# Optimization experiments

Measured on AMD Instinct MI355X. Metric: run time of the kernel, lower is better.

Reference implementation:

```python
import jax, jax.numpy as jnp
import numpy as np

STAGE = 100  # number of weight bins


def _bin_reconstruct(w, affine):
    # Faithful vectorization of the 100-iter binning loop: element in bin i
    # (half-open interval) gets scaled by affine[i]; the max element falls
    # outside every bin (w < wmin + stage*range/stage fails) and is zeroed.
    flat = w.reshape(-1)
    wmin, wmax = flat.min(), flat.max()
    idx = jnp.floor((flat - wmin) / (wmax - wmin) * STAGE).astype(jnp.int32)
    mask = (idx < STAGE).astype(flat.dtype)  # mask is detached in torch (non-diff anyway)
    scale = affine[jnp.clip(idx, 0, STAGE - 1)]
    return flat * scale * mask


def _kl_vs_laplace(new_flat, lap):
    # F.kl_div(log_softmax(w), softmax(lap), reduction='none').mean()
    logq = jax.nn.log_softmax(new_flat)
    p = jax.nn.softmax(lap)
    return (p * (jnp.log(p) - logq)).mean()


def _adder2d(x, w, stride, padding, groups=1):
    # AdderNet conv: out = -sum_k |patch_k - w_k| (no bias)
    O, Cg, kh, kw = w.shape
    patches = jax.lax.conv_general_dilated_patches(
        x, (kh, kw), (stride, stride), [(padding, padding), (padding, padding)])
    B, _, Hp, Wp = patches.shape  # channel dim ordered (C, kh, kw), C-major
    if groups == 1:
        p = patches.reshape(B, 1, Cg * kh * kw, Hp, Wp)
        wf = w.reshape(1, O, Cg * kh * kw, 1, 1)
    else:  # depthwise: groups == C_in, Cg == 1, O == C_in
        p = patches.reshape(B, O, kh * kw, Hp, Wp)
        wf = w.reshape(1, O, kh * kw, 1, 1)
    return -jnp.abs(p - wf).sum(axis=2)  # [B, O, Hp, Wp]


def _bn_train(x, g, b, eps=1e-5):
    # BatchNorm2d in training mode (batch statistics, biased variance)
    m = x.mean(axis=(0, 2, 3), keepdims=True)
    v = ((x - m) ** 2).mean(axis=(0, 2, 3), keepdims=True)
    return (x - m) * jax.lax.rsqrt(v + eps) * g.reshape(1, -1, 1, 1) + b.reshape(1, -1, 1, 1)


def _forward(x, sw_ds, sw_c1, sw_c2, sw_c3, a_ds, a_c1, a_c2, a_c3, peg_w,
             g1, b1, g2, b2, g3, b3, gds, bds, lap_ds, lap_c1, lap_c2, lap_c3):
    kl = jnp.float32(0.0)
    f_ds = _bin_reconstruct(sw_ds, a_ds)
    kl = kl + _kl_vs_laplace(f_ds, lap_ds)
    f_c1 = _bin_reconstruct(sw_c1, a_c1)
    kl = kl + _kl_vs_laplace(f_c1, lap_c1)
    residual = jax.nn.relu(_bn_train(_adder2d(x, f_ds.reshape(sw_ds.shape), 1, 0), gds, bds))
    h = _adder2d(x, f_c1.reshape(sw_c1.shape), 1, 0)
    h = _adder2d(h, peg_w, 1, 1, groups=peg_w.shape[0])  # PEG depthwise 3x3
    h = jax.nn.relu(_bn_train(h, g1, b1))
    f_c2 = _bin_reconstruct(sw_c2, a_c2)
    kl = kl + _kl_vs_laplace(f_c2, lap_c2)
    h = _adder2d(h, f_c2.reshape(sw_c2.shape), 1, 1)
    h = jax.nn.relu(_bn_train(h, g2, b2))
    f_c3 = _bin_reconstruct(sw_c3, a_c3)
    kl = kl + _kl_vs_laplace(f_c3, lap_c3)
    h = _adder2d(h, f_c3.reshape(sw_c3.shape), 1, 0)
    h = _bn_train(h, g3, b3)  # bn3 gamma zero-initialized
    return jax.nn.relu(h + residual), kl


def setup_inputs() -> dict:
    key = jax.random.key(0)
    ks = jax.random.split(key, 16)
    inp = {
        'x': jax.random.normal(ks[0], (4, 128, 28, 28), jnp.float32),
        'sw_downsample': jax.random.normal(ks[1], (256, 128, 1, 1), jnp.float32) * 0.05,
        'sw_conv1': jax.random.normal(ks[2], (64, 128, 1, 1), jnp.float32) * 0.05,
        'sw_conv2': jax.random.normal(ks[3], (64, 64, 3, 3), jnp.float32) * 0.05,
        'sw_conv3': jax.random.normal(ks[4], (256, 64, 1, 1), jnp.float32) * 0.05,
        'downsample_affine': jax.random.normal(ks[5], (100,), jnp.float32),
        'conv1_affine': jax.random.normal(ks[6], (100,), jnp.float32),
        'conv2_affine': jax.random.normal(ks[7], (100,), jnp.float32),
        'conv3_affine': jax.random.normal(ks[8], (100,), jnp.float32),
        'peg_w': jax.random.normal(ks[9], (64, 1, 3, 3), jnp.float32) * 0.05,
        'bn1_g': jnp.ones((64,), jnp.float32), 'bn1_b': jnp.zeros((64,), jnp.float32),
        'bn2_g': jnp.ones((64,), jnp.float32), 'bn2_b': jnp.zeros((64,), jnp.float32),
        'bn3_g': jnp.zeros((256,), jnp.float32), 'bn3_b': jnp.zeros((256,), jnp.float32),
        'bnds_g': jnp.ones((256,), jnp.float32), 'bnds_b': jnp.zeros((256,), jnp.float32),
        # Laplace(0, 2) samples, drawn once in setup so the reference is deterministic
        'lap_ds': jax.random.laplace(ks[10], (32768,), jnp.float32) * 2.0,
        'lap_c1': jax.random.laplace(ks[11], (8192,), jnp.float32) * 2.0,
        'lap_c2': jax.random.laplace(ks[12], (36864,), jnp.float32) * 2.0,
        'lap_c3': jax.random.laplace(ks[13], (16384,), jnp.float32) * 2.0,
    }
    return inp


def reference(x, sw_downsample, sw_conv1, sw_conv2, sw_conv3,
              downsample_affine, conv1_affine, conv2_affine, conv3_affine, peg_w,
              bn1_g, bn1_b, bn2_g, bn2_b, bn3_g, bn3_b, bnds_g, bnds_b,
              lap_ds, lap_c1, lap_c2, lap_c3):
    return _forward(x, sw_downsample, sw_conv1, sw_conv2, sw_conv3,
                    downsample_affine, conv1_affine, conv2_affine, conv3_affine, peg_w,
                    bn1_g, bn1_b, bn2_g, bn2_b, bn3_g, bn3_b, bnds_g, bnds_b,
                    lap_ds, lap_c1, lap_c2, lap_c3)
```

## Files before the change

kernel.cpp:

```cpp
#include <hip/hip_runtime.h>
#include <math.h>


#define HW 784
#define NB 4
#define STAGE 100

__device__ __forceinline__ float wredSum(float v){
  for (int o = 32; o > 0; o >>= 1) v += __shfl_down(v, o, 64);
  return v;
}
__device__ __forceinline__ float wredMax(float v){
  for (int o = 32; o > 0; o >>= 1) v = fmaxf(v, __shfl_down(v, o, 64));
  return v;
}
__device__ __forceinline__ float wredMin(float v){
  for (int o = 32; o > 0; o >>= 1) v = fminf(v, __shfl_down(v, o, 64));
  return v;
}
__device__ __forceinline__ double wredSumD(double v){
  for (int o = 32; o > 0; o >>= 1) v += __shfl_down(v, o, 64);
  return v;
}

__device__ float blockMin4(float v){
  __shared__ float shn[4];
  __syncthreads();
  v = wredMin(v);
  if ((threadIdx.x & 63) == 0) shn[threadIdx.x >> 6] = v;
  __syncthreads();
  return fminf(fminf(shn[0], shn[1]), fminf(shn[2], shn[3]));
}
__device__ float blockMax4(float v){
  __shared__ float shx[4];
  __syncthreads();
  v = wredMax(v);
  if ((threadIdx.x & 63) == 0) shx[threadIdx.x >> 6] = v;
  __syncthreads();
  return fmaxf(fmaxf(shx[0], shx[1]), fmaxf(shx[2], shx[3]));
}

__device__ void stats4(float v0, float v1, float v2, float v3,
                       double* sumP, double* sqP, int oc0){
  __shared__ double sred[4][8];
  __syncthreads();
  const int w = threadIdx.x >> 6;
  float vv[4] = {v0, v1, v2, v3};
  #pragma unroll
  for (int i = 0; i < 4; i++){
    double d = (double)vv[i];
    double s = wredSumD(d);
    double q = wredSumD(d * d);
    if ((threadIdx.x & 63) == 0){ sred[w][i] = s; sred[w][4 + i] = q; }
  }
  __syncthreads();
  if (threadIdx.x < 8){
    double tot = sred[0][threadIdx.x] + sred[1][threadIdx.x]
               + sred[2][threadIdx.x] + sred[3][threadIdx.x];
    int i = threadIdx.x & 3;
    if (threadIdx.x < 4) atomicAdd(&sumP[oc0 + i], tot);
    else                 atomicAdd(&sqP[oc0 + i],  tot);
  }
}
__device__ void stats2(float v0, float v1, double* sumP, double* sqP, int oc0){
  __shared__ double sred2[4][4];
  __syncthreads();
  const int w = threadIdx.x >> 6;
  float vv[2] = {v0, v1};
  #pragma unroll
  for (int i = 0; i < 2; i++){
    double d = (double)vv[i];
    double s = wredSumD(d);
    double q = wredSumD(d * d);
    if ((threadIdx.x & 63) == 0){ sred2[w][i] = s; sred2[w][2 + i] = q; }
  }
  __syncthreads();
  if (threadIdx.x < 4){
    double tot = sred2[0][threadIdx.x] + sred2[1][threadIdx.x]
               + sred2[2][threadIdx.x] + sred2[3][threadIdx.x];
    int i = threadIdx.x & 1;
    if (threadIdx.x < 2) atomicAdd(&sumP[oc0 + i], tot);
    else                 atomicAdd(&sqP[oc0 + i],  tot);
  }
}

__device__ void klAccum(float se, float sel, float sef, float sq, double* dst){
  __shared__ double kls[4][4];
  __syncthreads();
  const int w = threadIdx.x >> 6;
  double a0 = wredSumD((double)se);
  double a1 = wredSumD((double)sel);
  double a2 = wredSumD((double)sef);
  double a3 = wredSumD((double)sq);
  if ((threadIdx.x & 63) == 0){
    kls[w][0] = a0; kls[w][1] = a1; kls[w][2] = a2; kls[w][3] = a3;
  }
  __syncthreads();
  if (threadIdx.x < 4){
    double tot = kls[0][threadIdx.x] + kls[1][threadIdx.x]
               + kls[2][threadIdx.x] + kls[3][threadIdx.x];
    atomicAdd(&dst[threadIdx.x], tot);
  }
}

__device__ __forceinline__ float reconv(float vv, float mn, float rng,
                                        const float* saff){
  float q = (vv - mn) / rng * 100.0f;
  int idx = (int)floorf(q);
  float nv = 0.0f;
  if (idx < STAGE){
    int ci = idx < 0 ? 0 : (idx > STAGE - 1 ? STAGE - 1 : idx);
    nv = vv * saff[ci];
  }
  return nv;
}

__device__ __forceinline__ void mmReduce(const float* mmbuf, int tens,
                                         float& mn, float& mx){
  mn = 3.402823466e38f; mx = -3.402823466e38f;
  #pragma unroll
  for (int k = 0; k < 16; k++){
    mn = fminf(mn, mmbuf[tens * 32 + k]);
    mx = fmaxf(mx, mmbuf[tens * 32 + 16 + k]);
  }
}

__global__ __launch_bounds__(256) void minmax_kernel(
    const float* w0, int n0, const float* w1, int n1,
    const float* w2, int n2, const float* w3, int n3,
    float* mmbuf, double* dstat)
{
  if (threadIdx.x < 21) dstat[blockIdx.x * 21 + threadIdx.x] = 0.0;
  const int tens = blockIdx.x >> 4, slot = blockIdx.x & 15;
  const float* w; int n;
  if      (tens == 0){ w = w0; n = n0; }
  else if (tens == 1){ w = w1; n = n1; }
  else if (tens == 2){ w = w2; n = n2; }
  else               { w = w3; n = n3; }
  float mn = 3.402823466e38f, mx = -3.402823466e38f;
  for (int i = slot * 256 + threadIdx.x; i < n; i += 4096){
    float v = w[i];
    mn = fminf(mn, v); mx = fmaxf(mx, v);
  }
  mn = blockMin4(mn); mx = blockMax4(mx);
  if (threadIdx.x == 0){
    mmbuf[tens * 32 + slot]      = mn;
    mmbuf[tens * 32 + 16 + slot] = mx;
  }
}

__global__ __launch_bounds__(256) void front_kernel(
    const float* __restrict__ x,
    const float* __restrict__ w_ds, const float* __restrict__ aff_ds,
    const float* __restrict__ lap_ds,
    const float* __restrict__ w_c1, const float* __restrict__ aff_c1,
    const float* __restrict__ lap_c1,
    const float* __restrict__ w_c2, const float* __restrict__ aff_c2,
    const float* __restrict__ lap_c2, float* __restrict__ f_c2,
    const float* __restrict__ w_c3, const float* __restrict__ aff_c3,
    const float* __restrict__ lap_c3,
    const float* __restrict__ peg_w, const float* __restrict__ mmbuf,
    float* __restrict__ A, float* __restrict__ T2, double* __restrict__ dS)
{
  const int t = threadIdx.x;
  if (blockIdx.x < 512){
    const int a = blockIdx.x;
    const int chunk = a & 3, og = (a >> 2) & 31, b = a >> 7;
    const int oc0 = og * 8;
    __shared__ float saff[STAGE];
    __shared__ float sw[1024];
    if (t < STAGE) saff[t] = aff_ds[t];
    float mn, mx; mmReduce(mmbuf, 0, mn, mx);
    const float rng = mx - mn;
    __syncthreads();
    for (int k = t; k < 1024; k += 256)
      sw[k] = reconv(w_ds[oc0 * 128 + k], mn, rng, saff);
    __syncthreads();

    const int px = chunk * 196 + t;
    float v0=0,v1=0,v2=0,v3=0,v4=0,v5=0,v6=0,v7=0;
    if (t < 196){
      const float* xp = x + (size_t)b * 128 * HW + px;
      float c0=0,c1=0,c2=0,c3=0,c4=0,c5=0,c6=0,c7=0;
      #pragma unroll 4
      for (int c = 0; c < 128; c++){
        float xv = xp[(size_t)c * HW];
        c0 += fabsf(xv - sw[c]);
        c1 += fabsf(xv - sw[128 + c]);
        c2 += fabsf(xv - sw[256 + c]);
        c3 += fabsf(xv - sw[384 + c]);
        c4 += fabsf(xv - sw[512 + c]);
        c5 += fabsf(xv - sw[640 + c]);
        c6 += fabsf(xv - sw[768 + c]);
        c7 += fabsf(xv - sw[896 + c]);
      }
      v0=-c0; v1=-c1; v2=-c2; v3=-c3; v4=-c4; v5=-c5; v6=-c6; v7=-c7;
      float* op = A + ((size_t)(b * 256 + oc0)) * HW + px;
      op[0]=v0; op[HW]=v1; op[2*HW]=v2; op[3*HW]=v3;
      op[4*HW]=v4; op[5*HW]=v5; op[6*HW]=v6; op[7*HW]=v7;
    }
    stats4(v0, v1, v2, v3, dS + 0, dS + 256, oc0);
    stats4(v4, v5, v6, v7, dS + 0, dS + 256, oc0 + 4);

    if (b == 0 && chunk == 0){
      float se = 0, sel = 0, sef = 0, sq = 0;
      for (int k = t; k < 1024; k += 256){
        float l = lap_ds[oc0 * 128 + k];
        float e = expf(l);
        se += e; sel += e * l; sef += e * sw[k];
        sq += expf(sw[k]);
      }
      klAccum(se, sel, sef, sq, dS + 1280 + 0);
    }
  } else if (blockIdx.x < 768){
    const int a = blockIdx.x - 512;
    const int rc = a & 3, og = (a >> 2) & 15, b = a >> 6;
    const int oc0 = og * 4;
    __shared__ float saffc[STAGE];
    __shared__ float swc[512];
    __shared__ float swp[36];
    __shared__ float sT1[4][256];
    if (t < STAGE) saffc[t] = aff_c1[t];
    if (t >= 128 && t < 164) swp[t - 128] = peg_w[oc0 * 9 + (t - 128)];
    float mn, mx; mmReduce(mmbuf, 1, mn, mx);
    const float rng = mx - mn;
    __syncthreads();
    for (int k = t; k < 512; k += 256)
      swc[k] = reconv(w_c1[oc0 * 128 + k], mn, rng, saffc);
    __syncthreads();

    if (t < 252){
      const int rr = t / 28;
      const int col = t - rr * 28;
      const int wr = rc * 7 - 1 + rr;
      float tv0 = 0, tv1 = 0, tv2 = 0, tv3 = 0;
      if (wr >= 0 && wr < 28){
        const float* xp = x + (size_t)b * 128 * HW + wr * 28 + col;
        float c0 = 0, c1 = 0, c2 = 0, c3 = 0;
        #pragma unroll 4
        for (int c = 0; c < 128; c++){
          float xv = xp[(size_t)c * HW];
          c0 += fabsf(xv - swc[c]);
          c1 += fabsf(xv - swc[128 + c]);
          c2 += fabsf(xv - swc[256 + c]);
          c3 += fabsf(xv - swc[384 + c]);
        }
        tv0 = -c0; tv1 = -c1; tv2 = -c2; tv3 = -c3;
      }
      sT1[0][t] = tv0; sT1[1][t] = tv1; sT1[2][t] = tv2; sT1[3][t] = tv3;
    }
    __syncthreads();
    float v0 = 0, v1 = 0, v2 = 0, v3 = 0;
    if (t < 196){
      const int r = t / 28, col = t - r * 28;
      float c0 = 0, c1 = 0, c2 = 0, c3 = 0;
      #pragma unroll
      for (int ky = 0; ky < 3; ky++){
        #pragma unroll
        for (int kx = 0; kx < 3; kx++){
          int cc = col + kx - 1;
          bool ok = (cc >= 0) && (cc < 28);
          int idx = ok ? ((r + ky) * 28 + cc) : 0;
          float p0 = ok ? sT1[0][idx] : 0.0f;
          float p1 = ok ? sT1[1][idx] : 0.0f;
          float p2 = ok ? sT1[2][idx] : 0.0f;
          float p3 = ok ? sT1[3][idx] : 0.0f;
          int wk = ky * 3 + kx;
          c0 += fabsf(p0 - swp[wk]);
          c1 += fabsf(p1 - swp[9 + wk]);
          c2 += fabsf(p2 - swp[18 + wk]);
          c3 += fabsf(p3 - swp[27 + wk]);
        }
      }
      v0 = -c0; v1 = -c1; v2 = -c2; v3 = -c3;
      const int opx = (rc * 7 + r) * 28 + col;
      float* op = T2 + ((size_t)(b * 64 + oc0)) * HW + opx;
      op[0] = v0; op[HW] = v1; op[2 * HW] = v2; op[3 * HW] = v3;
    }
    stats4(v0, v1, v2, v3, dS + 512, dS + 576, oc0);

    if (b == 0 && rc == 0){
      float se = 0, sel = 0, sef = 0, sq = 0;
      for (int k = t; k < 512; k += 256){
        float l = lap_c1[oc0 * 128 + k];
        float e = expf(l);
        se += e; sel += e * l; sef += e * swc[k];
        sq += expf(swc[k]);
      }
      klAccum(se, sel, sef, sq, dS + 1280 + 4);
    }
  } else if (blockIdx.x < 832){
    const int j = blockIdx.x - 768;
    __shared__ float saff2[STAGE];
    if (t < STAGE) saff2[t] = aff_c2[t];
    float mn, mx; mmReduce(mmbuf, 2, mn, mx);
    const float rng = mx - mn;
    __syncthreads();
    float se = 0, sel = 0, sef = 0, sq = 0;
    for (int k = t; k < 576; k += 256){
      float nv = reconv(w_c2[j * 576 + k], mn, rng, saff2);
      f_c2[j * 576 + k] = nv;
      float l = lap_c2[j * 576 + k];
      float e = expf(l);
      se += e; sel += e * l; sef += e * nv; sq += expf(nv);
    }
    klAccum(se, sel, sef, sq, dS + 1280 + 8);
  } else {
    const int j = blockIdx.x - 832;
    __shared__ float saff3[STAGE];
    if (t < STAGE) saff3[t] = aff_c3[t];
    float mn, mx; mmReduce(mmbuf, 3, mn, mx);
    const float rng = mx - mn;
    __syncthreads();
    float se = 0, sel = 0, sef = 0, sq = 0;
    for (int k = t; k < 1024; k += 256){
      float nv = reconv(w_c3[j * 1024 + k], mn, rng, saff3);
      float l = lap_c3[j * 1024 + k];
      float e = expf(l);
      se += e; sel += e * l; sef += e * nv; sq += expf(nv);
    }
    klAccum(se, sel, sef, sq, dS + 1280 + 12);
  }
}

__global__ __launch_bounds__(256) void bnapply_pad_kernel(
    const float* __restrict__ T2, float* __restrict__ T2b,
    const float* __restrict__ g1, const float* __restrict__ b1,
    const double* __restrict__ dS)
{
  const int a = blockIdx.x;
  const int c = a & 63, b = a >> 6;
  __shared__ float ssc, ssb;
  if (threadIdx.x == 0){
    double s  = dS[512 + c] * (1.0 / 3136.0);
    double vr = dS[576 + c] * (1.0 / 3136.0) - s * s;
    float scale = g1[c] * rsqrtf((float)vr + 1e-5f);
    ssc = scale; ssb = b1[c] - (float)s * scale;
  }
  __syncthreads();
  const float sc_ = ssc, bi_ = ssb;
  const float* src = T2 + (size_t)a * HW;
  float* dst = T2b + (size_t)a * 960;
  for (int i = threadIdx.x; i < 960; i += 256){
    int row = i >> 5, col = i & 31;
    float v = 0.0f;
    if (row >= 1 && row <= 28 && col >= 1 && col <= 28)
      v = fmaxf(src[(row - 1) * 28 + (col - 1)] * sc_ + bi_, 0.0f);
    dst[i] = v;
  }
}

__global__ __launch_bounds__(256) void mid3x3_kernel(
    const float* __restrict__ T2b, const float* __restrict__ f_c2,
    float* __restrict__ T3, double* __restrict__ dS)
{
  const int t = threadIdx.x;
  const int a = blockIdx.x;
  const int chunk = a & 3, og = (a >> 2) & 31, b = a >> 7;
  const int oc0 = og * 2;
  const float* __restrict__ wA = f_c2 + oc0 * 576;
  const float* __restrict__ wB = wA + 576;

  float v0 = 0, v1 = 0;
  const int px = chunk * 196 + t;
  if (t < 196){
    const int y = px / 28, xc = px - y * 28;
    const float* base = T2b + (size_t)b * 64 * 960 + y * 32 + xc;
    float c0 = 0, c1 = 0;
    #pragma unroll 2
    for (int c = 0; c < 64; c++){
      const float* p = base + c * 960;
      float t0 = p[0],  t1 = p[1],  t2 = p[2];
      float t3 = p[32], t4 = p[33], t5 = p[34];
      float t6 = p[64], t7 = p[65], t8 = p[66];
      const float* wa = wA + c * 9;
      const float* wb = wB + c * 9;
      c0 += fabsf(t0 - wa[0]) + fabsf(t1 - wa[1]) + fabsf(t2 - wa[2])
          + fabsf(t3 - wa[3]) + fabsf(t4 - wa[4]) + fabsf(t5 - wa[5])
          + fabsf(t6 - wa[6]) + fabsf(t7 - wa[7]) + fabsf(t8 - wa[8]);
      c1 += fabsf(t0 - wb[0]) + fabsf(t1 - wb[1]) + fabsf(t2 - wb[2])
          + fabsf(t3 - wb[3]) + fabsf(t4 - wb[4]) + fabsf(t5 - wb[5])
          + fabsf(t6 - wb[6]) + fabsf(t7 - wb[7]) + fabsf(t8 - wb[8]);
    }
    v0 = -c0; v1 = -c1;
    T3[((size_t)(b * 64 + oc0)) * HW + px]     = v0;
    T3[((size_t)(b * 64 + oc0 + 1)) * HW + px] = v1;
  }
  stats2(v0, v1, dS + 640, dS + 704, oc0);
}

__global__ __launch_bounds__(256) void back_kernel(
    const float* __restrict__ T3, const float* __restrict__ w_c3,
    const float* __restrict__ aff_c3, const float* __restrict__ mmbuf,
    const float* __restrict__ g2, const float* __restrict__ b2,
    float* __restrict__ out, double* __restrict__ dS)
{
  const int t = threadIdx.x;
  const int a = blockIdx.x;
  const int chunk = a & 3, og = (a >> 2) & 63, b = a >> 8;
  const int oc0 = og * 4;
  __shared__ float ssc[64], ssb[64], sw[256], saff[STAGE];
  if (t < 64){
    double s  = dS[640 + t] * (1.0 / 3136.0);
    double vr = dS[704 + t] * (1.0 / 3136.0) - s * s;
    float scale = g2[t] * rsqrtf((float)vr + 1e-5f);
    ssc[t] = scale; ssb[t] = b2[t] - (float)s * scale;
  }
  if (t >= 128 && t < 128 + STAGE) saff[t - 128] = aff_c3[t - 128];
  float mn, mx; mmReduce(mmbuf, 3, mn, mx);
  const float rng = mx - mn;
  __syncthreads();
  sw[t] = reconv(w_c3[oc0 * 64 + t], mn, rng, saff);
  __syncthreads();

  const int px = chunk * 196 + t;
  float v0 = 0, v1 = 0, v2 = 0, v3 = 0;
  if (t < 196){
    const float* bp = T3 + (size_t)b * 64 * HW + px;
    float c0 = 0, c1 = 0, c2 = 0, c3 = 0;
    #pragma unroll 4
    for (int c = 0; c < 64; c++){
      float raw = bp[(size_t)c * HW];
      float vv = fmaxf(raw * ssc[c] + ssb[c], 0.0f);
      c0 += fabsf(vv - sw[c]);
      c1 += fabsf(vv - sw[64 + c]);
      c2 += fabsf(vv - sw[128 + c]);
      c3 += fabsf(vv - sw[192 + c]);
    }
    v0 = -c0; v1 = -c1; v2 = -c2; v3 = -c3;
    float* op = out + ((size_t)(b * 256 + oc0)) * HW + px;
    op[0] = v0; op[HW] = v1; op[2 * HW] = v2; op[3 * HW] = v3;
  }
  stats4(v0, v1, v2, v3, dS + 768, dS + 1024, oc0);
}

__global__ __launch_bounds__(256) void final_kernel(
    float* __restrict__ out, const float* __restrict__ A,
    const float* __restrict__ g3, const float* __restrict__ b3,
    const float* __restrict__ gds, const float* __restrict__ bds,
    const double* __restrict__ dS)
{
  __shared__ float s3c[256], s3b[256], sdc[256], sdb[256];
  const int t = threadIdx.x;
  {
    double s  = dS[768 + t] * (1.0 / 3136.0);
    double vr = dS[1024 + t] * (1.0 / 3136.0) - s * s;
    float scale = g3[t] * rsqrtf((float)vr + 1e-5f);
    s3c[t] = scale; s3b[t] = b3[t] - (float)s * scale;
    s  = dS[t] * (1.0 / 3136.0);
    vr = dS[256 + t] * (1.0 / 3136.0) - s * s;
    scale = gds[t] * rsqrtf((float)vr + 1e-5f);
    sdc[t] = scale; sdb[t] = bds[t] - (float)s * scale;
  }
  __syncthreads();
  #pragma unroll
  for (int k = 0; k < 4; k++){
    int n = blockIdx.x * 1024 + k * 256 + t;
    int c = (n / HW) & 255;
    float h = out[n], aa = A[n];
    float r = fmaxf(aa * sdc[c] + sdb[c], 0.0f);
    out[n] = fmaxf(h * s3c[c] + s3b[c] + r, 0.0f);
  }
  if (blockIdx.x == 0 && t == 0){
    const int ns[4] = {32768, 8192, 36864, 16384};
    float kl = 0.0f;
    #pragma unroll
    for (int q = 0; q < 4; q++){
      double se  = dS[1280 + q * 4];
      double sel = dS[1280 + q * 4 + 1];
      double sef = dS[1280 + q * 4 + 2];
      double sq  = dS[1280 + q * 4 + 3];
      kl += (float)((((sel - sef) / se) - log(se) + log(sq)) / (double)ns[q]);
    }
    out[802816] = kl;
  }
}

extern "C" void kernel_launch(void* const* d_in, const int* in_sizes, int n_in,
                              void* d_out, int out_size, void* d_ws, size_t ws_size,
                              hipStream_t stream)
{
  const float* x      = (const float*)d_in[0];
  const float* sw_ds  = (const float*)d_in[1];
  const float* sw_c1  = (const float*)d_in[2];
  const float* sw_c2  = (const float*)d_in[3];
  const float* sw_c3  = (const float*)d_in[4];
  const float* a_ds   = (const float*)d_in[5];
  const float* a_c1   = (const float*)d_in[6];
  const float* a_c2   = (const float*)d_in[7];
  const float* a_c3   = (const float*)d_in[8];
  const float* peg_w  = (const float*)d_in[9];
  const float* bn1_g  = (const float*)d_in[10];
  const float* bn1_b  = (const float*)d_in[11];
  const float* bn2_g  = (const float*)d_in[12];
  const float* bn2_b  = (const float*)d_in[13];
  const float* bn3_g  = (const float*)d_in[14];
  const float* bn3_b  = (const float*)d_in[15];
  const float* bnds_g = (const float*)d_in[16];
  const float* bnds_b = (const float*)d_in[17];
  const float* lap_ds = (const float*)d_in[18];
  const float* lap_c1 = (const float*)d_in[19];
  const float* lap_c2 = (const float*)d_in[20];
  const float* lap_c3 = (const float*)d_in[21];

  float* ws    = (float*)d_ws;
  float* f_c2  = ws;
  float* mmbuf = ws + 36864;
  double* dstat= (double*)(ws + 37120);
  float* A     = ws + 39808;
  float* T2    = ws + 842624;
  float* T3    = ws + 1043328;
  float* T2b   = ws + 1244032;

  float* out = (float*)d_out;

  minmax_kernel<<<64, 256, 0, stream>>>(
      sw_ds, 32768, sw_c1, 8192, sw_c2, 36864, sw_c3, 16384, mmbuf, dstat);

  front_kernel<<<848, 256, 0, stream>>>(
      x, sw_ds, a_ds, lap_ds, sw_c1, a_c1, lap_c1,
      sw_c2, a_c2, lap_c2, f_c2, sw_c3, a_c3, lap_c3,
      peg_w, mmbuf, A, T2, dstat);

  bnapply_pad_kernel<<<256, 256, 0, stream>>>(T2, T2b, bn1_g, bn1_b, dstat);

  mid3x3_kernel<<<512, 256, 0, stream>>>(T2b, f_c2, T3, dstat);

  back_kernel<<<1024, 256, 0, stream>>>(T3, sw_c3, a_c3, mmbuf,
                                        bn2_g, bn2_b, out, dstat);

  final_kernel<<<784, 256, 0, stream>>>(out, A, bn3_g, bn3_b, bnds_g, bnds_b,
                                        dstat);
}
```

Measured before the change: 171.3 us.

## Fuse BN-apply/pad into 3x3 adder conv and move downsample conv into mid kernel

Removes the separate bnapply_pad kernel. The 3x3 adder conv now loads T2 tiles into shared memory per 16-channel chunk, applying BN and ReLU with zero padding on the fly. The downsample 1x1 adder conv is moved out of the front kernel and runs as extra blocks of the new mid kernel. This lets the downsample branch overlap with the 3x3 conv and shortens the critical path before it. It saves one launch and the padded T2b round-trip through global memory, at the cost of redundant halo loads and more syncthreads per block.

```diff
diff --git a/kernel.cpp b/kernel.cpp
--- a/kernel.cpp
+++ b/kernel.cpp
@@ -151,8 +151,6 @@
 
 __global__ __launch_bounds__(256) void front_kernel(
     const float* __restrict__ x,
-    const float* __restrict__ w_ds, const float* __restrict__ aff_ds,
-    const float* __restrict__ lap_ds,
     const float* __restrict__ w_c1, const float* __restrict__ aff_c1,
     const float* __restrict__ lap_c1,
     const float* __restrict__ w_c2, const float* __restrict__ aff_c2,
@@ -160,60 +158,11 @@
     const float* __restrict__ w_c3, const float* __restrict__ aff_c3,
     const float* __restrict__ lap_c3,
     const float* __restrict__ peg_w, const float* __restrict__ mmbuf,
-    float* __restrict__ A, float* __restrict__ T2, double* __restrict__ dS)
+    float* __restrict__ T2, double* __restrict__ dS)
 {
   const int t = threadIdx.x;
-  if (blockIdx.x < 512){
+  if (blockIdx.x < 256){
     const int a = blockIdx.x;
-    const int chunk = a & 3, og = (a >> 2) & 31, b = a >> 7;
-    const int oc0 = og * 8;
-    __shared__ float saff[STAGE];
-    __shared__ float sw[1024];
-    if (t < STAGE) saff[t] = aff_ds[t];
-    float mn, mx; mmReduce(mmbuf, 0, mn, mx);
-    const float rng = mx - mn;
-    __syncthreads();
-    for (int k = t; k < 1024; k += 256)
-      sw[k] = reconv(w_ds[oc0 * 128 + k], mn, rng, saff);
-    __syncthreads();
-
-    const int px = chunk * 196 + t;
-    float v0=0,v1=0,v2=0,v3=0,v4=0,v5=0,v6=0,v7=0;
-    if (t < 196){
-      const float* xp = x + (size_t)b * 128 * HW + px;
-      float c0=0,c1=0,c2=0,c3=0,c4=0,c5=0,c6=0,c7=0;
-      #pragma unroll 4
-      for (int c = 0; c < 128; c++){
-        float xv = xp[(size_t)c * HW];
-        c0 += fabsf(xv - sw[c]);
-        c1 += fabsf(xv - sw[128 + c]);
-        c2 += fabsf(xv - sw[256 + c]);
-        c3 += fabsf(xv - sw[384 + c]);
-        c4 += fabsf(xv - sw[512 + c]);
-        c5 += fabsf(xv - sw[640 + c]);
-        c6 += fabsf(xv - sw[768 + c]);
-        c7 += fabsf(xv - sw[896 + c]);
-      }
-      v0=-c0; v1=-c1; v2=-c2; v3=-c3; v4=-c4; v5=-c5; v6=-c6; v7=-c7;
-      float* op = A + ((size_t)(b * 256 + oc0)) * HW + px;
-      op[0]=v0; op[HW]=v1; op[2*HW]=v2; op[3*HW]=v3;
-      op[4*HW]=v4; op[5*HW]=v5; op[6*HW]=v6; op[7*HW]=v7;
-    }
-    stats4(v0, v1, v2, v3, dS + 0, dS + 256, oc0);
-    stats4(v4, v5, v6, v7, dS + 0, dS + 256, oc0 + 4);
-
-    if (b == 0 && chunk == 0){
-      float se = 0, sel = 0, sef = 0, sq = 0;
-      for (int k = t; k < 1024; k += 256){
-        float l = lap_ds[oc0 * 128 + k];
-        float e = expf(l);
-        se += e; sel += e * l; sef += e * sw[k];
-        sq += expf(sw[k]);
-      }
-      klAccum(se, sel, sef, sq, dS + 1280 + 0);
-    }
-  } else if (blockIdx.x < 768){
-    const int a = blockIdx.x - 512;
     const int rc = a & 3, og = (a >> 2) & 15, b = a >> 6;
     const int oc0 = og * 4;
     __shared__ float saffc[STAGE];
@@ -289,8 +238,8 @@
       }
       klAccum(se, sel, sef, sq, dS + 1280 + 4);
     }
-  } else if (blockIdx.x < 832){
-    const int j = blockIdx.x - 768;
+  } else if (blockIdx.x < 320){
+    const int j = blockIdx.x - 256;
     __shared__ float saff2[STAGE];
     if (t < STAGE) saff2[t] = aff_c2[t];
     float mn, mx; mmReduce(mmbuf, 2, mn, mx);
@@ -306,7 +255,7 @@
     }
     klAccum(se, sel, sef, sq, dS + 1280 + 8);
   } else {
-    const int j = blockIdx.x - 832;
+    const int j = blockIdx.x - 320;
     __shared__ float saff3[STAGE];
     if (t < STAGE) saff3[t] = aff_c3[t];
     float mn, mx; mmReduce(mmbuf, 3, mn, mx);
@@ -323,70 +272,131 @@
   }
 }
 
-__global__ __launch_bounds__(256) void bnapply_pad_kernel(
-    const float* __restrict__ T2, float* __restrict__ T2b,
+__global__ __launch_bounds__(256) void mid_kernel(
+    const float* __restrict__ x,
+    const float* __restrict__ T2, const float* __restrict__ f_c2,
     const float* __restrict__ g1, const float* __restrict__ b1,
-    const double* __restrict__ dS)
-{
-  const int a = blockIdx.x;
-  const int c = a & 63, b = a >> 6;
-  __shared__ float ssc, ssb;
-  if (threadIdx.x == 0){
-    double s  = dS[512 + c] * (1.0 / 3136.0);
-    double vr = dS[576 + c] * (1.0 / 3136.0) - s * s;
-    float scale = g1[c] * rsqrtf((float)vr + 1e-5f);
-    ssc = scale; ssb = b1[c] - (float)s * scale;
-  }
-  __syncthreads();
-  const float sc_ = ssc, bi_ = ssb;
-  const float* src = T2 + (size_t)a * HW;
-  float* dst = T2b + (size_t)a * 960;
-  for (int i = threadIdx.x; i < 960; i += 256){
-    int row = i >> 5, col = i & 31;
-    float v = 0.0f;
-    if (row >= 1 && row <= 28 && col >= 1 && col <= 28)
-      v = fmaxf(src[(row - 1) * 28 + (col - 1)] * sc_ + bi_, 0.0f);
-    dst[i] = v;
-  }
-}
-
-__global__ __launch_bounds__(256) void mid3x3_kernel(
-    const float* __restrict__ T2b, const float* __restrict__ f_c2,
-    float* __restrict__ T3, double* __restrict__ dS)
+    const float* __restrict__ w_ds, const float* __restrict__ aff_ds,
+    const float* __restrict__ lap_ds, const float* __restrict__ mmbuf,
+    float* __restrict__ T3, float* __restrict__ A, double* __restrict__ dS)
 {
   const int t = threadIdx.x;
-  const int a = blockIdx.x;
-  const int chunk = a & 3, og = (a >> 2) & 31, b = a >> 7;
-  const int oc0 = og * 2;
-  const float* __restrict__ wA = f_c2 + oc0 * 576;
-  const float* __restrict__ wB = wA + 576;
-
-  float v0 = 0, v1 = 0;
-  const int px = chunk * 196 + t;
-  if (t < 196){
-    const int y = px / 28, xc = px - y * 28;
-    const float* base = T2b + (size_t)b * 64 * 960 + y * 32 + xc;
-    float c0 = 0, c1 = 0;
-    #pragma unroll 2
-    for (int c = 0; c < 64; c++){
-      const float* p = base + c * 960;
-      float t0 = p[0],  t1 = p[1],  t2 = p[2];
-      float t3 = p[32], t4 = p[33], t5 = p[34];
-      float t6 = p[64], t7 = p[65], t8 = p[66];
-      const float* wa = wA + c * 9;
-      const float* wb = wB + c * 9;
-      c0 += fabsf(t0 - wa[0]) + fabsf(t1 - wa[1]) + fabsf(t2 - wa[2])
-          + fabsf(t3 - wa[3]) + fabsf(t4 - wa[4]) + fabsf(t5 - wa[5])
-          + fabsf(t6 - wa[6]) + fabsf(t7 - wa[7]) + fabsf(t8 - wa[8]);
-      c1 += fabsf(t0 - wb[0]) + fabsf(t1 - wb[1]) + fabsf(t2 - wb[2])
-          + fabsf(t3 - wb[3]) + fabsf(t4 - wb[4]) + fabsf(t5 - wb[5])
-          + fabsf(t6 - wb[6]) + fabsf(t7 - wb[7]) + fabsf(t8 - wb[8]);
-    }
-    v0 = -c0; v1 = -c1;
-    T3[((size_t)(b * 64 + oc0)) * HW + px]     = v0;
-    T3[((size_t)(b * 64 + oc0 + 1)) * HW + px] = v1;
-  }
-  stats2(v0, v1, dS + 640, dS + 704, oc0);
+  if (blockIdx.x < 512){
+    const int a = blockIdx.x;
+    const int chunk = a & 3, og = (a >> 2) & 31, b = a >> 7;
+    const int oc0 = og * 2;
+    __shared__ float ssc[64], ssb[64];
+    __shared__ float sT[16 * 288];
+    if (t < 64){
+      double s  = dS[512 + t] * (1.0 / 3136.0);
+      double vr = dS[576 + t] * (1.0 / 3136.0) - s * s;
+      float scale = g1[t] * rsqrtf((float)vr + 1e-5f);
+      ssc[t] = scale; ssb[t] = b1[t] - (float)s * scale;
+    }
+    const float* __restrict__ wA = f_c2 + oc0 * 576;
+    const float* __restrict__ wB = wA + 576;
+    const int r = t / 28;
+    const int col = t - r * 28;
+    const int row0 = chunk * 7;
+    float c0acc = 0.0f, c1acc = 0.0f;
+
+    for (int cc = 0; cc < 4; cc++){
+      const int cbase = cc * 16;
+      __syncthreads();
+      #pragma unroll
+      for (int k = 0; k < 18; k++){
+        int i = t + k * 256;
+        int cl = i & 31;
+        int rem = i >> 5;
+        int c_local = rem / 9;
+        int rr = rem - c_local * 9;
+        int wr = row0 - 1 + rr;
+        int wc = cl - 1;
+        float v = 0.0f;
+        if (wr >= 0 && wr < 28 && wc >= 0 && wc < 28){
+          int c = cbase + c_local;
+          float raw = T2[((size_t)(b * 64 + c)) * HW + wr * 28 + wc];
+          v = fmaxf(raw * ssc[c] + ssb[c], 0.0f);
+        }
+        sT[i] = v;
+      }
+      __syncthreads();
+      if (t < 196){
+        #pragma unroll 2
+        for (int c = 0; c < 16; c++){
+          const float* p = sT + c * 288 + r * 32 + col;
+          float t0 = p[0],  t1 = p[1],  t2 = p[2];
+          float t3 = p[32], t4 = p[33], t5 = p[34];
+          float t6 = p[64], t7 = p[65], t8 = p[66];
+          const float* wa = wA + (cbase + c) * 9;
+          const float* wb = wB + (cbase + c) * 9;
+          c0acc += fabsf(t0 - wa[0]) + fabsf(t1 - wa[1]) + fabsf(t2 - wa[2])
+                 + fabsf(t3 - wa[3]) + fabsf(t4 - wa[4]) + fabsf(t5 - wa[5])
+                 + fabsf(t6 - wa[6]) + fabsf(t7 - wa[7]) + fabsf(t8 - wa[8]);
+          c1acc += fabsf(t0 - wb[0]) + fabsf(t1 - wb[1]) + fabsf(t2 - wb[2])
+                 + fabsf(t3 - wb[3]) + fabsf(t4 - wb[4]) + fabsf(t5 - wb[5])
+                 + fabsf(t6 - wb[6]) + fabsf(t7 - wb[7]) + fabsf(t8 - wb[8]);
+        }
+      }
+    }
+    float v0 = 0.0f, v1 = 0.0f;
+    if (t < 196){
+      v0 = -c0acc; v1 = -c1acc;
+      const int px = chunk * 196 + t;
+      T3[((size_t)(b * 64 + oc0)) * HW + px]     = v0;
+      T3[((size_t)(b * 64 + oc0 + 1)) * HW + px] = v1;
+    }
+    stats2(v0, v1, dS + 640, dS + 704, oc0);
+  } else {
+    const int a = blockIdx.x - 512;
+    const int chunk = a & 3, og = (a >> 2) & 31, b = a >> 7;
+    const int oc0 = og * 8;
+    __shared__ float saff[STAGE];
+    __shared__ float sw[1024];
+    if (t < STAGE) saff[t] = aff_ds[t];
+    float mn, mx; mmReduce(mmbuf, 0, mn, mx);
+    const float rng = mx - mn;
+    __syncthreads();
+    for (int k = t; k < 1024; k += 256)
+      sw[k] = reconv(w_ds[oc0 * 128 + k], mn, rng, saff);
+    __syncthreads();
+
+    const int px = chunk * 196 + t;
+    float v0=0,v1=0,v2=0,v3=0,v4=0,v5=0,v6=0,v7=0;
+    if (t < 196){
+      const float* xp = x + (size_t)b * 128 * HW + px;
+      float c0=0,c1=0,c2=0,c3=0,c4=0,c5=0,c6=0,c7=0;
+      #pragma unroll 4
+      for (int c = 0; c < 128; c++){
+        float xv = xp[(size_t)c * HW];
+        c0 += fabsf(xv - sw[c]);
+        c1 += fabsf(xv - sw[128 + c]);
+        c2 += fabsf(xv - sw[256 + c]);
+        c3 += fabsf(xv - sw[384 + c]);
+        c4 += fabsf(xv - sw[512 + c]);
+        c5 += fabsf(xv - sw[640 + c]);
+        c6 += fabsf(xv - sw[768 + c]);
+        c7 += fabsf(xv - sw[896 + c]);
+      }
+      v0=-c0; v1=-c1; v2=-c2; v3=-c3; v4=-c4; v5=-c5; v6=-c6; v7=-c7;
+      float* op = A + ((size_t)(b * 256 + oc0)) * HW + px;
+      op[0]=v0; op[HW]=v1; op[2*HW]=v2; op[3*HW]=v3;
+      op[4*HW]=v4; op[5*HW]=v5; op[6*HW]=v6; op[7*HW]=v7;
+    }
+    stats4(v0, v1, v2, v3, dS + 0, dS + 256, oc0);
+    stats4(v4, v5, v6, v7, dS + 0, dS + 256, oc0 + 4);
+
+    if (b == 0 && chunk == 0){
+      float se = 0, sel = 0, sef = 0, sq = 0;
+      for (int k = t; k < 1024; k += 256){
+        float l = lap_ds[oc0 * 128 + k];
+        float e = expf(l);
+        se += e; sel += e * l; sef += e * sw[k];
+        sq += expf(sw[k]);
+      }
+      klAccum(se, sel, sef, sq, dS + 1280 + 0);
+    }
+  }
 }
 
 __global__ __launch_bounds__(256) void back_kernel(
@@ -510,21 +520,18 @@
   float* A     = ws + 39808;
   float* T2    = ws + 842624;
   float* T3    = ws + 1043328;
-  float* T2b   = ws + 1244032;
 
   float* out = (float*)d_out;
 
   minmax_kernel<<<64, 256, 0, stream>>>(
       sw_ds, 32768, sw_c1, 8192, sw_c2, 36864, sw_c3, 16384, mmbuf, dstat);
 
-  front_kernel<<<848, 256, 0, stream>>>(
-      x, sw_ds, a_ds, lap_ds, sw_c1, a_c1, lap_c1,
-      sw_c2, a_c2, lap_c2, f_c2, sw_c3, a_c3, lap_c3,
-      peg_w, mmbuf, A, T2, dstat);
-
-  bnapply_pad_kernel<<<256, 256, 0, stream>>>(T2, T2b, bn1_g, bn1_b, dstat);
-
-  mid3x3_kernel<<<512, 256, 0, stream>>>(T2b, f_c2, T3, dstat);
+  front_kernel<<<336, 256, 0, stream>>>(
+      x, sw_c1, a_c1, lap_c1, sw_c2, a_c2, lap_c2, f_c2,
+      sw_c3, a_c3, lap_c3, peg_w, mmbuf, T2, dstat);
+
+  mid_kernel<<<1024, 256, 0, stream>>>(
+      x, T2, f_c2, bn1_g, bn1_b, sw_ds, a_ds, lap_ds, mmbuf, T3, A, dstat);
 
   back_kernel<<<1024, 256, 0, stream>>>(T3, sw_c3, a_c3, mmbuf,
                                         bn2_g, bn2_b, out, dstat);
```

After: 180.1 us. +5.1%, slower.
